# Optimization experiments

Measured on AMD Instinct MI355X. Metric: run time of the kernel, lower is better.

## Reference

```python
import jax, jax.numpy as jnp
import numpy as np

DIM = 2048
NUM_HEADS = 16
NUM_KV_HEADS = 4
HEAD_DIM = DIM // NUM_HEADS
KV_DIM = NUM_KV_HEADS * HEAD_DIM
ROPE_BASE = 10000.0
QK_GAIN_INIT = 1.0
BSZ, SEQ = 4, 2048


def rms_norm(x):
    eps = jnp.finfo(x.dtype).eps
    return x * jax.lax.rsqrt(jnp.mean(x * x, axis=-1, keepdims=True) + eps)


def rope_cos_sin(seqlen, head_dim, base, dtype):
    inv_freq = base ** (-jnp.arange(0, head_dim, 2, dtype=jnp.float32) / head_dim)
    t = jnp.arange(seqlen, dtype=jnp.float32)
    freqs = t[:, None] * inv_freq[None, :]  # [S, hd/2]
    return jnp.cos(freqs).astype(dtype), jnp.sin(freqs).astype(dtype)


def apply_rotary(x, cos, sin):
    # x: [B, H, S, hd]; cos/sin: [S, hd/2]
    x1, x2 = jnp.split(x, 2, axis=-1)
    c = cos[None, None, :, :]
    s = sin[None, None, :, :]
    return jnp.concatenate([x1 * c + x2 * s, -x1 * s + x2 * c], axis=-1)


def setup_inputs() -> dict:
    key = jax.random.key(0)
    ks = jax.random.split(key, 6)
    std = 0.02
    return {
        "x": jax.random.normal(ks[0], (BSZ, SEQ, DIM), dtype=jnp.float32),
        "Wq": jax.random.normal(ks[1], (DIM, DIM), dtype=jnp.float32) * std,
        "Wk": jax.random.normal(ks[2], (KV_DIM, DIM), dtype=jnp.float32) * std,
        "Wv": jax.random.normal(ks[3], (KV_DIM, DIM), dtype=jnp.float32) * std,
        "Wo": jax.random.normal(ks[4], (DIM, DIM), dtype=jnp.float32) * std,
        "q_gain": jnp.full((NUM_HEADS,), QK_GAIN_INIT, dtype=jnp.float32),
    }


def reference(x, Wq, Wk, Wv, Wo, q_gain):
    bsz, seqlen, dim = x.shape
    # QKV projections (F.linear: x @ W.T)
    q = (x @ Wq.T).reshape(bsz, seqlen, NUM_HEADS, HEAD_DIM).transpose(0, 2, 1, 3)
    k = (x @ Wk.T).reshape(bsz, seqlen, NUM_KV_HEADS, HEAD_DIM).transpose(0, 2, 1, 3)
    v = (x @ Wv.T).reshape(bsz, seqlen, NUM_KV_HEADS, HEAD_DIM).transpose(0, 2, 1, 3)
    # QK RMSNorm
    q = rms_norm(q)
    k = rms_norm(k)
    # RoPE
    cos, sin = rope_cos_sin(seqlen, HEAD_DIM, ROPE_BASE, q.dtype)
    q = apply_rotary(q, cos, sin)
    k = apply_rotary(k, cos, sin)
    # per-head gain
    q = q * q_gain.astype(q.dtype)[None, :, None, None]
    # GQA: repeat kv heads
    rep = NUM_HEADS // NUM_KV_HEADS
    k = jnp.repeat(k, rep, axis=1)
    v = jnp.repeat(v, rep, axis=1)
    # causal SDPA
    scale = 1.0 / jnp.sqrt(jnp.asarray(HEAD_DIM, dtype=q.dtype))
    scores = jnp.einsum("bhsd,bhtd->bhst", q, k) * scale
    causal = jnp.tril(jnp.ones((seqlen, seqlen), dtype=bool))
    scores = jnp.where(causal[None, None], scores, jnp.asarray(-jnp.inf, scores.dtype))
    attn = jax.nn.softmax(scores, axis=-1)
    y = jnp.einsum("bhst,bhtd->bhsd", attn, v)
    y = y.transpose(0, 2, 1, 3).reshape(bsz, seqlen, dim)
    return y @ Wo.T
```

## Files before the change

kernel.cpp:

```cpp
#include <hip/hip_runtime.h>
#include <hip/hip_bf16.h>

typedef __hip_bfloat16 bf16;
typedef short s16x8 __attribute__((ext_vector_type(8)));
typedef float f32x4 __attribute__((ext_vector_type(4)));
typedef unsigned int u32x4 __attribute__((ext_vector_type(4)));

#define DIM 2048
#define NHEADS 16
#define NKVH 4
#define HD 128
#define KVDIM 512
#define BSZ 4
#define SEQ 2048
#define MROWS (BSZ*SEQ)
#define NQKV (DIM+2*KVDIM)

__device__ __forceinline__ void gld_lds16(const bf16* g, short* l) {
  __builtin_amdgcn_global_load_lds((__attribute__((address_space(1))) void*)(void*)g,
                                   (__attribute__((address_space(3))) void*)l, 16, 0, 0);
}

__device__ __forceinline__ void nts16(void* p, uint4 v) {
  u32x4 w = {v.x, v.y, v.z, v.w};
  __builtin_nontemporal_store(w, (u32x4*)p);
}
__device__ __forceinline__ void nts8(void* p, unsigned long long v) {
  __builtin_nontemporal_store(v, (unsigned long long*)p);
}
__device__ __forceinline__ void nts16f(void* p, float4 v) {
  f32x4 w = {v.x, v.y, v.z, v.w};
  __builtin_nontemporal_store(w, (f32x4*)p);
}
__device__ __forceinline__ void nts2(void* p, bf16 v) {
  __builtin_nontemporal_store(*(short*)&v, (short*)p);
}

__global__ __launch_bounds__(256) void cast_all(
    const float* __restrict__ x,  const float* __restrict__ Wq,
    const float* __restrict__ Wk, const float* __restrict__ Wv,
    const float* __restrict__ Wo, bf16* __restrict__ xbf,
    bf16* __restrict__ Wqkv, bf16* __restrict__ Wob) {
  const int i = blockIdx.x*256 + threadIdx.x;
  const float* src; bf16* dst; int j, o;
  if (i < 2097152)      { src = x;  dst = xbf;  j = i;           o = i; }
  else if (i < 2621440) { src = Wq; dst = Wqkv; j = i - 2097152; o = i - 2097152; }
  else if (i < 2752512) { src = Wk; dst = Wqkv; j = i - 2621440; o = i - 2097152; }
  else if (i < 2883584) { src = Wv; dst = Wqkv; j = i - 2752512; o = i - 2097152; }
  else                  { src = Wo; dst = Wob;  j = i - 2883584; o = i - 2883584; }
  const float4* s4 = (const float4*)src;
  float4 a = s4[2*j];
  float4 b = s4[2*j+1];
  union { bf16 h[8]; uint4 u; } pk;
  pk.h[0] = __float2bfloat16(a.x); pk.h[1] = __float2bfloat16(a.y);
  pk.h[2] = __float2bfloat16(a.z); pk.h[3] = __float2bfloat16(a.w);
  pk.h[4] = __float2bfloat16(b.x); pk.h[5] = __float2bfloat16(b.y);
  pk.h[6] = __float2bfloat16(b.z); pk.h[7] = __float2bfloat16(b.w);
  nts16(((uint4*)dst) + o, pk.u);
}


template<int MQ>
__device__ __forceinline__ void lda(s16x8 (&af)[4][2], const short* pa, int rds) {
#pragma unroll
  for (int fr = 0; fr < 4; fr++)
#pragma unroll
    for (int ks = 0; ks < 2; ks++)
      af[fr][ks] = *(const s16x8*)(pa + ((MQ*4 + fr)*2 + ks)*512 + rds);
}
template<int NQ>
__device__ __forceinline__ void ldb(s16x8 (&bfv)[2][2], const short* pb, int bsub, int rds) {
#pragma unroll
  for (int fc = 0; fc < 2; fc++)
#pragma unroll
    for (int ks = 0; ks < 2; ks++)
      bfv[fc][ks] = *(const s16x8*)(pb + (bsub + (NQ*2 + fc)*2 + ks)*512 + rds);
}
template<int MQ, int NQ>
__device__ __forceinline__ void mmq(f32x4 (&acc)[8][4], const s16x8 (&af)[4][2],
                                    const s16x8 (&bfv)[2][2]) {
#pragma unroll
  for (int fr = 0; fr < 4; fr++)
#pragma unroll
    for (int fc = 0; fc < 2; fc++)
#pragma unroll
      for (int ks = 0; ks < 2; ks++)
        acc[MQ*4+fr][NQ*2+fc] = __builtin_amdgcn_mfma_f32_16x16x32_bf16(
            af[fr][ks], bfv[fc][ks], acc[MQ*4+fr][NQ*2+fc], 0, 0, 0);
}

#define WV6 asm volatile("s_waitcnt vmcnt(6)" ::: "memory")
#define WV0 asm volatile("s_waitcnt vmcnt(0)" ::: "memory")
#define WVN ((void)0)
#define GBAR __builtin_amdgcn_s_barrier()
#define WLK asm volatile("s_waitcnt lgkmcnt(0)" ::: "memory")
#define PRI1 __builtin_amdgcn_s_setprio(1)
#define PRI0 __builtin_amdgcn_s_setprio(0)

#define KT(B_, T_, S1_, S2_, WVX) do {                                          \
    const short* pa = pAr[B_];                                                  \
    const short* pb = pBr[B_];                                                  \
    s16x8 af[4][2], b0f[2][2], b1f[2][2];                                       \
                                                        \
    lda<0>(af, pa, rds); ldb<0>(b0f, pb, bsub, rds);                            \
    if (S1_) {                                                                  \
      gld_lds16(Ab +      (long)((T_)+1)*64 + eA1, &L[1-(B_)][0][4096+wid512]); \
      gld_lds16(Ab + h1 + (long)((T_)+1)*64 + eA1, &L[1-(B_)][1][4096+wid512]); \
    }                                                                           \
    GBAR; WLK; PRI1; mmq<0,0>(acc, af, b0f); PRI0; GBAR;                        \
                                                        \
    ldb<1>(b1f, pb, bsub, rds);                                                 \
    if (S2_) {                                                                  \
      gld_lds16(Ab +      (long)((T_)+2)*64 + eA0, &L[B_][0][wid512]);          \
      gld_lds16(Ab + h1 + (long)((T_)+2)*64 + eA0, &L[B_][1][wid512]);          \
    }                                                                           \
    GBAR; WLK; PRI1; mmq<0,1>(acc, af, b1f); PRI0; GBAR;                        \
                                                        \
    lda<1>(af, pa, rds);                                                        \
    if (S2_) {                                                                  \
      gld_lds16(Bb + (long)((T_)+2)*64 + eA0, &L[B_][2][wid512]);               \
      gld_lds16(Bb + (long)((T_)+2)*64 + eA1, &L[B_][2][4096+wid512]);          \
    }                                                                           \
    GBAR; WLK; PRI1; mmq<1,0>(acc, af, b0f); PRI0; GBAR;                        \
                                                        \
    if (S2_) {                                                                  \
      gld_lds16(Bb + h1 + (long)((T_)+2)*64 + eA0, &L[B_][3][wid512]);          \
      gld_lds16(Bb + h1 + (long)((T_)+2)*64 + eA1, &L[B_][3][4096+wid512]);     \
    }                                                                           \
    WVX;                                                                        \
    GBAR; PRI1; mmq<1,1>(acc, af, b1f); PRI0; GBAR;                             \
  } while (0)

template<int EPI>
__global__ __launch_bounds__(512, 2) void gemm8(
    const bf16* __restrict__ A, const bf16* __restrict__ Bm,
    float* __restrict__ Cf, bf16* __restrict__ Qo, bf16* __restrict__ Ko,
    bf16* __restrict__ Vo, const float* __restrict__ gain, int N, int K) {
  __shared__ short L[2][4][8192] __attribute__((aligned(16)));
  const int tid = threadIdx.x;
  const int lane = tid & 63, wid = tid >> 6;
  const int quad = lane >> 4, l15 = lane & 15;
  const int wm = wid >> 2, wn = wid & 3;

  const int gx  = gridDim.x;
  const int lin = blockIdx.y * gx + blockIdx.x;
  const int cpx = (gx * gridDim.y) >> 3;
  const int swz = (lin & 7) * cpx + (lin >> 3);
  const int m0 = (swz / gx) * 256, n0 = (swz % gx) * 256;

  const int rds = l15*32 + ((quad*8) ^ ((l15 & 8) << 1));
  const int bsub = (wn & 1) * 8;

  const int colx = ((lane & 3) * 8) ^ ((lane >> 5) << 4);
  const int gc   = ((wid & 1) << 5) + colx;
  const int gr0  = ((wid >> 1) << 4) + (lane >> 2);
  const long eA0 = (long)gr0 * K + gc;
  const long eA1 = eA0 + 64L * K;
  const int wid512 = wid * 512;
  const bf16* Ab = A  + (long)m0 * K;
  const bf16* Bb = Bm + (long)n0 * K;
  const long h1 = 128L * K;

  const short* pAr[2] = { &L[0][wm][0], &L[1][wm][0] };
  const short* pBr[2] = { &L[0][2 + (wn >> 1)][0], &L[1][2 + (wn >> 1)][0] };

  f32x4 acc[8][4] = {};

  gld_lds16(Ab + eA0,           &L[0][0][wid512]);
  gld_lds16(Ab + eA1,           &L[0][0][4096 + wid512]);
  gld_lds16(Ab + h1 + eA0,      &L[0][1][wid512]);
  gld_lds16(Ab + h1 + eA1,      &L[0][1][4096 + wid512]);
  gld_lds16(Bb + eA0,           &L[0][2][wid512]);
  gld_lds16(Bb + eA1,           &L[0][2][4096 + wid512]);
  gld_lds16(Bb + h1 + eA0,      &L[0][3][wid512]);
  gld_lds16(Bb + h1 + eA1,      &L[0][3][4096 + wid512]);
  gld_lds16(Ab + 64 + eA0,      &L[1][0][wid512]);
  gld_lds16(Ab + h1 + 64 + eA0, &L[1][1][wid512]);
  gld_lds16(Bb + 64 + eA0,      &L[1][2][wid512]);
  gld_lds16(Bb + 64 + eA1,      &L[1][2][4096 + wid512]);
  gld_lds16(Bb + h1 + 64 + eA0, &L[1][3][wid512]);
  gld_lds16(Bb + h1 + 64 + eA1, &L[1][3][4096 + wid512]);
  WV6;
  GBAR;

  for (int t = 0; t < 30; t += 2) {
    KT(0, t,   1, 1, WV6);
    KT(1, t+1, 1, 1, WV6);
  }
  KT(0, 30, 1, 0, WV0);
  KT(1, 31, 0, 0, WVN);

  const int colg0 = n0 + wn*64;
  const int bb = (m0 + wm*128) >> 11;
  const int sb = (m0 + wm*128) & (SEQ-1);
  if (EPI == 0) {
    float* ew = (float*)(&L[0][0][0]) + wid*4096;
    const int rowb = m0 + wm*128;
    const int rr = lane >> 3, c4 = (lane & 7)*4;
#pragma unroll
    for (int half = 0; half < 2; half++) {
#pragma unroll
      for (int mi = 0; mi < 8; mi++)
#pragma unroll
        for (int nj2 = 0; nj2 < 2; nj2++)
#pragma unroll
          for (int r = 0; r < 4; r++)
            ew[(mi*16 + quad*4 + r)*32 + nj2*16 + l15] = acc[mi][half*2 + nj2][r];
      asm volatile("" ::: "memory");
#pragma unroll
      for (int it = 0; it < 16; it++) {
        const int row = it*8 + rr;
        float4 v = *(const float4*)&ew[row*32 + c4];
        nts16f(Cf + (long)(rowb + row)*N + colg0 + half*32 + c4, v);
      }
      asm volatile("" ::: "memory");
    }
  } else if (n0 >= DIM + KVDIM) {
    const int cv = colg0 - (DIM + KVDIM);
    const int h  = cv >> 7;
    const int db = cv & 127;
    bf16* vb = Vo + ((long)(bb*NKVH + h)*HD)*SEQ + sb;
#pragma unroll
    for (int mi = 0; mi < 8; mi++)
#pragma unroll
      for (int nj = 0; nj < 4; nj++) {
        const int d = db + nj*16 + l15;
        union { bf16 h4[4]; unsigned long long u; } pk;
        pk.h4[0] = __float2bfloat16(acc[mi][nj][0]);
        pk.h4[1] = __float2bfloat16(acc[mi][nj][1]);
        pk.h4[2] = __float2bfloat16(acc[mi][nj][2]);
        pk.h4[3] = __float2bfloat16(acc[mi][nj][3]);
        nts8(vb + (long)d*SEQ + mi*16 + quad*4, pk.u);
      }
  } else {
    short* Ls = &L[0][0][0];
    short* rw = Ls + (wm*2 + (wn >> 1))*16384;
    const int cw = (wn & 1)*64;
#pragma unroll
    for (int mi = 0; mi < 8; mi++)
#pragma unroll
      for (int nj = 0; nj < 4; nj++)
#pragma unroll
        for (int r = 0; r < 4; r++) {
          bf16 hv = __float2bfloat16(acc[mi][nj][r]);
          rw[(mi*16 + quad*4 + r)*128 + cw + nj*16 + l15] = *(short*)&hv;
        }
    __syncthreads();
    const int h2 = wn >> 1;
    const short* rg = Ls + (wm*2 + h2)*16384;
    const int row0 = (wn & 1)*64;
    float g; bf16* gb;
    if (n0 < DIM) {
      const int h = (n0 >> 7) + h2;
      g = gain[h] * 0.08838834764831845f;
      gb = Qo + (long)(bb*NHEADS + h)*SEQ*HD;
    } else {
      const int h = ((n0 - DIM) >> 7) + h2;
      g = 1.0f;
      gb = Ko + (long)(bb*NKVH + h)*SEQ*HD;
    }
    const float inv_freq = exp2f((float)lane * -0.20762050593046014f);
    for (int rI = 0; rI < 64; rI++) {
      const int row = row0 + rI;
      const float x1 = __bfloat162float(*(const bf16*)&rg[row*128 + lane]);
      const float x2 = __bfloat162float(*(const bf16*)&rg[row*128 + 64 + lane]);
      float ss = x1*x1 + x2*x2;
#pragma unroll
      for (int off = 1; off < 64; off <<= 1) ss += __shfl_xor(ss, off);
      const float rn = rsqrtf(ss*(1.0f/128.0f) + 1.1920928955078125e-07f);
      const int s = sb + row;
      float sn, cs;
      sincosf((float)s * inv_freq, &sn, &cs);
      const float q1 = x1*rn, q2 = x2*rn;
      bf16* pr = gb + (long)s*HD;
      nts2(pr + lane,      __float2bfloat16((q1*cs + q2*sn)*g));
      nts2(pr + 64 + lane, __float2bfloat16((q2*cs - q1*sn)*g));
    }
  }
}

__global__ __launch_bounds__(256, 2) void attn(
    const bf16* __restrict__ Qb, const bf16* __restrict__ Kb,
    const bf16* __restrict__ Vtg, bf16* __restrict__ Yb) {
  __shared__ short Kt[64*136]  __attribute__((aligned(16)));
  __shared__ short Vt[128*72]  __attribute__((aligned(16)));
  __shared__ short Pt[4*2304]  __attribute__((aligned(16)));

  const int tid = threadIdx.x;
  const int lane = tid & 63, wid = tid >> 6;
  const int quad = lane >> 4, l15 = lane & 15;
  const int lin = blockIdx.y*8 + blockIdx.x;
  const int swz = (lin & 7)*64 + (lin >> 3);
  const int xb = swz & 7;
  const int bh = swz >> 3;
  const int b = bh >> 4, h = bh & 15, kvh = h >> 2;

  const bf16* kbase = Kb  + (long)(b*NKVH + kvh)*SEQ*HD;
  const bf16* vbase = Vtg + (long)(b*NKVH + kvh)*HD*SEQ;
  short* pw0 = Pt + wid*2304;
  short* pw1 = pw0 + 1152;
  const int krow = tid >> 4, kc = (tid & 15)*8;
  const int vrow = tid >> 3, vc = (tid & 7)*8;

#define LOADK(KT_) do {                                                        \
    kr0 = *(const uint4*)(kbase + (long)((KT_)*64 +  0 + krow)*HD + kc);       \
    kr1 = *(const uint4*)(kbase + (long)((KT_)*64 + 16 + krow)*HD + kc);       \
    kr2 = *(const uint4*)(kbase + (long)((KT_)*64 + 32 + krow)*HD + kc);       \
    kr3 = *(const uint4*)(kbase + (long)((KT_)*64 + 48 + krow)*HD + kc);       \
  } while (0)
#define LOADV(KT_) do {                                                        \
    vr0 = *(const uint4*)(vbase + (long)(  0 + vrow)*SEQ + (KT_)*64 + vc);     \
    vr1 = *(const uint4*)(vbase + (long)( 32 + vrow)*SEQ + (KT_)*64 + vc);     \
    vr2 = *(const uint4*)(vbase + (long)( 64 + vrow)*SEQ + (KT_)*64 + vc);     \
    vr3 = *(const uint4*)(vbase + (long)( 96 + vrow)*SEQ + (KT_)*64 + vc);     \
  } while (0)

  for (int phase = 0; phase < 2; phase++) {
    const int qt = phase ? xb : (15 - xb);
    const int q0 = qt*128 + wid*16 + l15;
    const int q1 = q0 + 64;
    const bf16* qr0 = Qb + ((long)(b*NHEADS + h)*SEQ + q0)*HD + quad*8;
    s16x8 qa0[4], qa1[4];
#pragma unroll
    for (int st = 0; st < 4; st++) {
      qa0[st] = *(const s16x8*)(qr0 + st*32);
      qa1[st] = *(const s16x8*)(qr0 + 64*HD + st*32);
    }

    f32x4 o0[8] = {}, o1[8] = {};
    float li0 = 0.0f, li1 = 0.0f;
    const int ktiles = 2*qt + 2;

    uint4 kr0, kr1, kr2, kr3, vr0, vr1, vr2, vr3;
    LOADK(0); LOADV(0);

    for (int kt = 0; kt < ktiles; kt++) {
      __syncthreads();
      *(uint4*)&Kt[( 0 + krow)*136 + kc] = kr0;
      *(uint4*)&Kt[(16 + krow)*136 + kc] = kr1;
      *(uint4*)&Kt[(32 + krow)*136 + kc] = kr2;
      *(uint4*)&Kt[(48 + krow)*136 + kc] = kr3;
      *(uint4*)&Vt[(  0 + vrow)*72 + vc] = vr0;
      *(uint4*)&Vt[( 32 + vrow)*72 + vc] = vr1;
      *(uint4*)&Vt[( 64 + vrow)*72 + vc] = vr2;
      *(uint4*)&Vt[( 96 + vrow)*72 + vc] = vr3;
      __syncthreads();
      if (kt + 1 < ktiles) { LOADK(kt+1); LOADV(kt+1); }

      f32x4 s0[4] = {}, s1[4] = {};
#pragma unroll
      for (int nt = 0; nt < 4; nt++) {
        s16x8 kf[4];
#pragma unroll
        for (int st = 0; st < 4; st++)
          kf[st] = *(const s16x8*)&Kt[(nt*16 + l15)*136 + st*32 + quad*8];
        PRI1;
#pragma unroll
        for (int st = 0; st < 4; st++) {
          s0[nt] = __builtin_amdgcn_mfma_f32_16x16x32_bf16(kf[st], qa0[st], s0[nt], 0, 0, 0);
          s1[nt] = __builtin_amdgcn_mfma_f32_16x16x32_bf16(kf[st], qa1[st], s1[nt], 0, 0, 0);
        }
        PRI0;
      }

      const bool d0 = (kt >= 2*qt);
      const bool d1 = (kt >  2*qt);
      const int tb = kt*64 + quad*4;
      union { bf16 h[16]; unsigned long long u[4]; } p0, p1;
      float rs0 = 0.0f, rs1 = 0.0f;
#pragma unroll
      for (int nt = 0; nt < 4; nt++) {
#pragma unroll
        for (int r = 0; r < 4; r++) {
          const int t = tb + nt*16 + r;
          float v0 = s0[nt][r], v1 = s1[nt][r];
          if (d0 && (t > q0)) v0 = -1e30f;
          if (d1 && (t > q1)) v1 = -1e30f;
          const float e0 = __expf(v0 - 12.0f);
          const float e1 = __expf(v1 - 12.0f);
          rs0 += e0; rs1 += e1;
          p0.h[nt*4+r] = __float2bfloat16(e0);
          p1.h[nt*4+r] = __float2bfloat16(e1);
        }
      }
      li0 += rs0; li1 += rs1;
#pragma unroll
      for (int nt = 0; nt < 4; nt++) {
        *(unsigned long long*)&pw0[l15*72 + nt*16 + quad*4] = p0.u[nt];
        *(unsigned long long*)&pw1[l15*72 + nt*16 + quad*4] = p1.u[nt];
      }

#pragma unroll
      for (int st = 0; st < 2; st++) {
        s16x8 pf0 = *(const s16x8*)&pw0[l15*72 + st*32 + quad*8];
        s16x8 pf1 = *(const s16x8*)&pw1[l15*72 + st*32 + quad*8];
        PRI1;
#pragma unroll
        for (int dt = 0; dt < 8; dt++) {
          s16x8 vf = *(const s16x8*)&Vt[(dt*16 + l15)*72 + st*32 + quad*8];
          o0[dt] = __builtin_amdgcn_mfma_f32_16x16x32_bf16(vf, pf0, o0[dt], 0, 0, 0);
          o1[dt] = __builtin_amdgcn_mfma_f32_16x16x32_bf16(vf, pf1, o1[dt], 0, 0, 0);
        }
        PRI0;
      }
    }

    li0 += __shfl_xor(li0, 16); li0 += __shfl_xor(li0, 32);
    li1 += __shfl_xor(li1, 16); li1 += __shfl_xor(li1, 32);
    const float inv0 = 1.0f / li0, inv1 = 1.0f / li1;

    short* ep = pw0;
#pragma unroll
    for (int g = 0; g < 2; g++) {
      const float inv = g ? inv1 : inv0;
      const f32x4* o = g ? o1 : o0;
      const int qg = g ? q1 : q0;
#pragma unroll
      for (int dt = 0; dt < 8; dt++) {
        union { bf16 h[4]; unsigned long long u; } pk;
        pk.h[0] = __float2bfloat16(o[dt][0]*inv);
        pk.h[1] = __float2bfloat16(o[dt][1]*inv);
        pk.h[2] = __float2bfloat16(o[dt][2]*inv);
        pk.h[3] = __float2bfloat16(o[dt][3]*inv);
        *(unsigned long long*)&ep[l15*136 + dt*16 + quad*4] = pk.u;
      }
      bf16* yb = Yb + ((long)(b*SEQ + qg - l15))*DIM + h*HD;
#pragma unroll
      for (int p = 0; p < 4; p++) {
        const int c = quad + 4*p;
        uint4 yv = *(const uint4*)&ep[l15*136 + c*8];
        nts16(&yb[(long)l15*DIM + c*8], yv);
      }
    }
  }
#undef LOADK
#undef LOADV
}

extern "C" void kernel_launch(void* const* d_in, const int* in_sizes, int n_in,
                              void* d_out, int out_size, void* d_ws, size_t ws_size,
                              hipStream_t stream) {
  (void)in_sizes; (void)n_in; (void)out_size; (void)ws_size;
  const float* x   = (const float*)d_in[0];
  const float* Wq  = (const float*)d_in[1];
  const float* Wk  = (const float*)d_in[2];
  const float* Wv  = (const float*)d_in[3];
  const float* Wo  = (const float*)d_in[4];
  const float* qg  = (const float*)d_in[5];

  char* ws = (char*)d_ws;
  bf16* xbf  = (bf16*)(ws);
  bf16* Wqkv = (bf16*)(ws + 33554432);
  bf16* Wob  = (bf16*)(ws + 46137344);
  bf16* Qb   = (bf16*)(ws + 54525952);
  bf16* Kb   = (bf16*)(ws + 88080384);
  bf16* Vb   = (bf16*)(ws + 96468992);
  bf16* Yb   = (bf16*)(ws + 104857600);

  cast_all<<<13312, 256, 0, stream>>>(x, Wq, Wk, Wv, Wo, xbf, Wqkv, Wob);

  gemm8<1><<<dim3(NQKV/256, MROWS/256), 512, 0, stream>>>(
      xbf, Wqkv, nullptr, Qb, Kb, Vb, qg, NQKV, DIM);

  attn<<<dim3(8, BSZ*NHEADS), 256, 0, stream>>>(Qb, Kb, Vb, Yb);

  gemm8<0><<<dim3(DIM/256, MROWS/256), 512, 0, stream>>>(
      Yb, Wob, (float*)d_out, nullptr, nullptr, nullptr, nullptr, DIM, DIM);
}
```

Before: 468.2 us.

## Precompute RoPE table, reduce QK norm from accumulators, drop nontemporal stores

The cast kernel now also fills a cos/sin table for every position and frequency. The QKV GEMM epilogue reads that table instead of calling sincosf per row. The RMS sum of squares is computed from the fp32 accumulators with 16-lane shuffles and shared memory, replacing a 64-lane shuffle reduction per row. All nontemporal stores become plain stores. The table reuses the Y buffer region, which is safe only because attention overwrites Y after the QKV GEMM has consumed the table. The norm now uses fp32 accumulator values rather than the bf16-rounded ones.

```diff
diff --git a/kernel.cpp b/kernel.cpp
--- a/kernel.cpp
+++ b/kernel.cpp
@@ -4,7 +4,6 @@
 typedef __hip_bfloat16 bf16;
 typedef short s16x8 __attribute__((ext_vector_type(8)));
 typedef float f32x4 __attribute__((ext_vector_type(4)));
-typedef unsigned int u32x4 __attribute__((ext_vector_type(4)));
 
 #define DIM 2048
 #define NHEADS 16
@@ -21,27 +20,21 @@
                                    (__attribute__((address_space(3))) void*)l, 16, 0, 0);
 }
 
-__device__ __forceinline__ void nts16(void* p, uint4 v) {
-  u32x4 w = {v.x, v.y, v.z, v.w};
-  __builtin_nontemporal_store(w, (u32x4*)p);
-}
-__device__ __forceinline__ void nts8(void* p, unsigned long long v) {
-  __builtin_nontemporal_store(v, (unsigned long long*)p);
-}
-__device__ __forceinline__ void nts16f(void* p, float4 v) {
-  f32x4 w = {v.x, v.y, v.z, v.w};
-  __builtin_nontemporal_store(w, (f32x4*)p);
-}
-__device__ __forceinline__ void nts2(void* p, bf16 v) {
-  __builtin_nontemporal_store(*(short*)&v, (short*)p);
-}
-
 __global__ __launch_bounds__(256) void cast_all(
     const float* __restrict__ x,  const float* __restrict__ Wq,
     const float* __restrict__ Wk, const float* __restrict__ Wv,
     const float* __restrict__ Wo, bf16* __restrict__ xbf,
-    bf16* __restrict__ Wqkv, bf16* __restrict__ Wob) {
+    bf16* __restrict__ Wqkv, bf16* __restrict__ Wob,
+    float2* __restrict__ tab) {
   const int i = blockIdx.x*256 + threadIdx.x;
+  if (i >= 3407872) {
+    const int i2 = i - 3407872;
+    const int s = i2 >> 6, d = i2 & 63;
+    float sn, cs;
+    sincosf((float)s * exp2f((float)d * -0.20762050593046014f), &sn, &cs);
+    tab[i2] = make_float2(cs, sn);
+    return;
+  }
   const float* src; bf16* dst; int j, o;
   if (i < 2097152)      { src = x;  dst = xbf;  j = i;           o = i; }
   else if (i < 2621440) { src = Wq; dst = Wqkv; j = i - 2097152; o = i - 2097152; }
@@ -56,7 +49,7 @@
   pk.h[2] = __float2bfloat16(a.z); pk.h[3] = __float2bfloat16(a.w);
   pk.h[4] = __float2bfloat16(b.x); pk.h[5] = __float2bfloat16(b.y);
   pk.h[6] = __float2bfloat16(b.z); pk.h[7] = __float2bfloat16(b.w);
-  nts16(((uint4*)dst) + o, pk.u);
+  ((uint4*)dst)[o] = pk.u;
 }
 
 
@@ -135,8 +128,10 @@
 __global__ __launch_bounds__(512, 2) void gemm8(
     const bf16* __restrict__ A, const bf16* __restrict__ Bm,
     float* __restrict__ Cf, bf16* __restrict__ Qo, bf16* __restrict__ Ko,
-    bf16* __restrict__ Vo, const float* __restrict__ gain, int N, int K) {
+    bf16* __restrict__ Vo, const float* __restrict__ gain,
+    const float2* __restrict__ tab, int N, int K) {
   __shared__ short L[2][4][8192] __attribute__((aligned(16)));
+  __shared__ float rs[4][2][128];
   const int tid = threadIdx.x;
   const int lane = tid & 63, wid = tid >> 6;
   const int quad = lane >> 4, l15 = lane & 15;
@@ -211,7 +206,7 @@
       for (int it = 0; it < 16; it++) {
         const int row = it*8 + rr;
         float4 v = *(const float4*)&ew[row*32 + c4];
-        nts16f(Cf + (long)(rowb + row)*N + colg0 + half*32 + c4, v);
+        *(float4*)(Cf + (long)(rowb + row)*N + colg0 + half*32 + c4) = v;
       }
       asm volatile("" ::: "memory");
     }
@@ -230,12 +225,34 @@
         pk.h4[1] = __float2bfloat16(acc[mi][nj][1]);
         pk.h4[2] = __float2bfloat16(acc[mi][nj][2]);
         pk.h4[3] = __float2bfloat16(acc[mi][nj][3]);
-        nts8(vb + (long)d*SEQ + mi*16 + quad*4, pk.u);
+        *(unsigned long long*)(vb + (long)d*SEQ + mi*16 + quad*4) = pk.u;
       }
   } else {
+    float p[8][4];
+#pragma unroll
+    for (int mi = 0; mi < 8; mi++)
+#pragma unroll
+      for (int r = 0; r < 4; r++) {
+        float v = acc[mi][0][r]*acc[mi][0][r];
+        v += acc[mi][1][r]*acc[mi][1][r];
+        v += acc[mi][2][r]*acc[mi][2][r];
+        v += acc[mi][3][r]*acc[mi][3][r];
+#pragma unroll
+        for (int off = 1; off < 16; off <<= 1) v += __shfl_xor(v, off);
+        p[mi][r] = v;
+      }
+    const int reg = wm*2 + (wn >> 1);
+    const int half = wn & 1;
+    if (l15 == 0) {
+#pragma unroll
+      for (int mi = 0; mi < 8; mi++)
+#pragma unroll
+        for (int r = 0; r < 4; r++)
+          rs[reg][half][mi*16 + quad*4 + r] = p[mi][r];
+    }
     short* Ls = &L[0][0][0];
-    short* rw = Ls + (wm*2 + (wn >> 1))*16384;
-    const int cw = (wn & 1)*64;
+    short* rw = Ls + reg*16384;
+    const int cw = half*64;
 #pragma unroll
     for (int mi = 0; mi < 8; mi++)
 #pragma unroll
@@ -246,35 +263,30 @@
           rw[(mi*16 + quad*4 + r)*128 + cw + nj*16 + l15] = *(short*)&hv;
         }
     __syncthreads();
-    const int h2 = wn >> 1;
-    const short* rg = Ls + (wm*2 + h2)*16384;
-    const int row0 = (wn & 1)*64;
+    const short* rg = Ls + reg*16384;
+    const int row0 = half*64;
     float g; bf16* gb;
     if (n0 < DIM) {
-      const int h = (n0 >> 7) + h2;
+      const int h = (n0 >> 7) + (wn >> 1);
       g = gain[h] * 0.08838834764831845f;
       gb = Qo + (long)(bb*NHEADS + h)*SEQ*HD;
     } else {
-      const int h = ((n0 - DIM) >> 7) + h2;
+      const int h = ((n0 - DIM) >> 7) + (wn >> 1);
       g = 1.0f;
       gb = Ko + (long)(bb*NKVH + h)*SEQ*HD;
     }
-    const float inv_freq = exp2f((float)lane * -0.20762050593046014f);
     for (int rI = 0; rI < 64; rI++) {
       const int row = row0 + rI;
       const float x1 = __bfloat162float(*(const bf16*)&rg[row*128 + lane]);
       const float x2 = __bfloat162float(*(const bf16*)&rg[row*128 + 64 + lane]);
-      float ss = x1*x1 + x2*x2;
-#pragma unroll
-      for (int off = 1; off < 64; off <<= 1) ss += __shfl_xor(ss, off);
-      const float rn = rsqrtf(ss*(1.0f/128.0f) + 1.1920928955078125e-07f);
+      const float ssum = rs[reg][0][row] + rs[reg][1][row];
+      const float rn = rsqrtf(ssum*(1.0f/128.0f) + 1.1920928955078125e-07f);
       const int s = sb + row;
-      float sn, cs;
-      sincosf((float)s * inv_freq, &sn, &cs);
+      const float2 cs = tab[s*64 + lane];
       const float q1 = x1*rn, q2 = x2*rn;
       bf16* pr = gb + (long)s*HD;
-      nts2(pr + lane,      __float2bfloat16((q1*cs + q2*sn)*g));
-      nts2(pr + 64 + lane, __float2bfloat16((q2*cs - q1*sn)*g));
+      pr[lane]      = __float2bfloat16((q1*cs.x + q2*cs.y)*g);
+      pr[64 + lane] = __float2bfloat16((q2*cs.x - q1*cs.y)*g);
     }
   }
 }
@@ -429,7 +441,7 @@
       for (int p = 0; p < 4; p++) {
         const int c = quad + 4*p;
         uint4 yv = *(const uint4*)&ep[l15*136 + c*8];
-        nts16(&yb[(long)l15*DIM + c*8], yv);
+        *(uint4*)&yb[(long)l15*DIM + c*8] = yv;
       }
     }
   }
@@ -456,14 +468,15 @@
   bf16* Kb   = (bf16*)(ws + 88080384);
   bf16* Vb   = (bf16*)(ws + 96468992);
   bf16* Yb   = (bf16*)(ws + 104857600);
-
-  cast_all<<<13312, 256, 0, stream>>>(x, Wq, Wk, Wv, Wo, xbf, Wqkv, Wob);
+  float2* tab = (float2*)(ws + 104857600);
+
+  cast_all<<<13824, 256, 0, stream>>>(x, Wq, Wk, Wv, Wo, xbf, Wqkv, Wob, tab);
 
   gemm8<1><<<dim3(NQKV/256, MROWS/256), 512, 0, stream>>>(
-      xbf, Wqkv, nullptr, Qb, Kb, Vb, qg, NQKV, DIM);
+      xbf, Wqkv, nullptr, Qb, Kb, Vb, qg, tab, NQKV, DIM);
 
   attn<<<dim3(8, BSZ*NHEADS), 256, 0, stream>>>(Qb, Kb, Vb, Yb);
 
   gemm8<0><<<dim3(DIM/256, MROWS/256), 512, 0, stream>>>(
-      Yb, Wob, (float*)d_out, nullptr, nullptr, nullptr, nullptr, DIM, DIM);
-}
+      Yb, Wob, (float*)d_out, nullptr, nullptr, nullptr, nullptr, nullptr, DIM, DIM);
+}
```

New measurement: 439.1 us. 6.2% less time.
